# Kernel tuning notes

Hardware: AMD Instinct MI355X
Metric: run time of the kernel (lower is better)

Reference implementation:

```python
import jax, jax.numpy as jnp
import numpy as np

# Longformer-base-4096 dims; attention_window=128 -> one-sided window 64
B, S, D, H, L, F, V, NUM_LABELS = 1, 4096, 768, 12, 12, 3072, 50265, 100
DH = D // H
W = 64            # one-sided sliding window
NC = S // W       # number of query chunks
EPS = 1e-5
SCALE = float(1.0 / np.sqrt(DH))


def layer_norm(x, s, b):
    m = jnp.mean(x, axis=-1, keepdims=True)
    v = jnp.mean(jnp.square(x - m), axis=-1, keepdims=True)
    return (x - m) * jax.lax.rsqrt(v + EPS) * s + b


def heads(x):  # [B,S,D] -> [B,H,S,DH]
    return x.reshape(B, S, H, DH).transpose(0, 2, 1, 3)


def chunk3(t):  # [B,H,S,DH] -> [B,H,NC,3W,DH]: key blocks c-1,c,c+1 per query chunk c
    tp = jnp.pad(t, ((0, 0), (0, 0), (W, W), (0, 0)))
    tb = tp.reshape(B, H, NC + 2, W, DH)
    return jnp.concatenate([tb[:, :, i:i + NC] for i in range(3)], axis=3)


def _forward(input_ids, attention_mask, emb_tok, emb_pos, ln_emb_scale, ln_emb_bias,
             Wq, bq, Wk, bk, Wv, bv, Wqg, bqg, Wkg, bkg, Wvg, bvg, Wo, bo,
             ln1_scale, ln1_bias, Wf1, bf1, Wf2, bf2, ln2_scale, ln2_bias, Wc, bc):
    am = attention_mask > 0                      # [B,S]
    x = layer_norm(emb_tok[input_ids] + emb_pos[None, :, :], ln_emb_scale, ln_emb_bias)

    # static sliding-window masks, shared by all layers
    qi = jnp.arange(W)[:, None]
    kj = jnp.arange(3 * W)[None, :]
    band = (kj >= qi) & (kj <= qi + 2 * W)       # |key - query| <= W within a chunk triple
    kvalid = am & (jnp.arange(S)[None, :] > 0)   # global token (pos 0) excluded from window
    kp = jnp.pad(kvalid, ((0, 0), (W, W))).reshape(B, NC + 2, W)
    kmask = jnp.concatenate([kp[:, i:i + NC] for i in range(3)], axis=2)   # [B,NC,3W]
    win_mask = band[None, None, None] & kmask[:, None, :, None, :]         # [B,1,NC,W,3W]

    def layer(x, p):
        (wq, bq_, wk, bk_, wv, bv_, wqg, bqg_, wkg, bkg_, wvg, bvg_, wo, bo_,
         l1s, l1b, wf1, bf1_, wf2, bf2_, l2s, l2b) = p
        q = heads(x @ wq + bq_) * SCALE
        k = heads(x @ wk + bk_)
        v = heads(x @ wv + bv_)
        qc = q.reshape(B, H, NC, W, DH)
        k3, v3 = chunk3(k), chunk3(v)
        sc = jnp.einsum('bhcqd,bhckd->bhcqk', qc, k3)          # [B,H,NC,W,3W]
        sc = jnp.where(win_mask, sc, -1e9)
        # every token also attends to the global CLS key (standard K/V of pos 0)
        sg = jnp.einsum('bhsd,bhd->bhs', q, k[:, :, 0]).reshape(B, H, NC, W, 1)
        probs = jax.nn.softmax(jnp.concatenate([sg, sc], axis=-1), axis=-1)
        pg, pl = probs[..., 0], probs[..., 1:]
        ctx = jnp.einsum('bhcqk,bhckd->bhcqd', pl, v3).reshape(B, H, S, DH)
        ctx = ctx + pg.reshape(B, H, S, 1) * v[:, :, :1]
        # global token attends to everything with its own (global) projections
        qg = heads(x @ wqg + bqg_)[:, :, 0] * SCALE            # [B,H,DH]
        kg = heads(x @ wkg + bkg_)
        vg = heads(x @ wvg + bvg_)
        sgl = jnp.where(am[:, None, :], jnp.einsum('bhd,bhjd->bhj', qg, kg), -1e9)
        ctx0 = jnp.einsum('bhj,bhjd->bhd', jax.nn.softmax(sgl, axis=-1), vg)
        ctx = ctx.at[:, :, 0].set(ctx0)
        attn = ctx.transpose(0, 2, 1, 3).reshape(B, S, D) @ wo + bo_
        x1 = layer_norm(x + attn, l1s, l1b)
        h = jax.nn.gelu(x1 @ wf1 + bf1_, approximate=False)
        return layer_norm(x1 + h @ wf2 + bf2_, l2s, l2b), None

    params = (Wq, bq, Wk, bk, Wv, bv, Wqg, bqg, Wkg, bkg, Wvg, bvg, Wo, bo,
              ln1_scale, ln1_bias, Wf1, bf1, Wf2, bf2, ln2_scale, ln2_bias)
    x, _ = jax.lax.scan(layer, x, params)
    return x[:, 0] @ Wc + bc                                   # [B, NUM_LABELS]


def setup_inputs():
    key = jax.random.key(0)
    ks = jax.random.split(key, 40)
    it = iter(range(40))
    nrm = lambda shape: jax.random.normal(ks[next(it)], shape, dtype=jnp.float32) * 0.02
    z = lambda shape: jnp.zeros(shape, jnp.float32)
    o = lambda shape: jnp.ones(shape, jnp.float32)
    return {
        'input_ids': jax.random.randint(ks[next(it)], (B, S), 0, V, dtype=jnp.int32),
        'attention_mask': jnp.ones((B, S), dtype=jnp.int32),
        'emb_tok': nrm((V, D)), 'emb_pos': nrm((S, D)),
        'ln_emb_scale': o((D,)), 'ln_emb_bias': z((D,)),
        'Wq': nrm((L, D, D)), 'bq': z((L, D)),
        'Wk': nrm((L, D, D)), 'bk': z((L, D)),
        'Wv': nrm((L, D, D)), 'bv': z((L, D)),
        'Wqg': nrm((L, D, D)), 'bqg': z((L, D)),
        'Wkg': nrm((L, D, D)), 'bkg': z((L, D)),
        'Wvg': nrm((L, D, D)), 'bvg': z((L, D)),
        'Wo': nrm((L, D, D)), 'bo': z((L, D)),
        'ln1_scale': o((L, D)), 'ln1_bias': z((L, D)),
        'Wf1': nrm((L, D, F)), 'bf1': z((L, F)),
        'Wf2': nrm((L, F, D)), 'bf2': z((L, D)),
        'ln2_scale': o((L, D)), 'ln2_bias': z((L, D)),
        'Wc': nrm((D, NUM_LABELS)), 'bc': z((NUM_LABELS,)),
    }


def reference(input_ids, attention_mask, emb_tok, emb_pos, ln_emb_scale, ln_emb_bias,
              Wq, bq, Wk, bk, Wv, bv, Wqg, bqg, Wkg, bkg, Wvg, bvg, Wo, bo,
              ln1_scale, ln1_bias, Wf1, bf1, Wf2, bf2, ln2_scale, ln2_bias, Wc, bc):
    return _forward(input_ids, attention_mask, emb_tok, emb_pos, ln_emb_scale, ln_emb_bias,
                    Wq, bq, Wk, bk, Wv, bv, Wqg, bqg, Wkg, bkg, Wvg, bvg, Wo, bo,
                    ln1_scale, ln1_bias, Wf1, bf1, Wf2, bf2, ln2_scale, ln2_bias, Wc, bc)
```

## Files before the change

kernel.cpp:

```cpp
#include <hip/hip_runtime.h>
#include <hip/hip_bf16.h>

typedef unsigned short u16;
typedef __attribute__((ext_vector_type(8))) short bf16x8;
typedef __attribute__((ext_vector_type(4))) float f32x4;

constexpr int S = 4096, D = 768, H = 12, NL = 12, F = 3072, NLAB = 100, DH = 64;
constexpr int NQKV = 3840;
constexpr float SCALE = 0.125f;
constexpr float EPS = 1e-5f;

__device__ __forceinline__ float bits2f(u16 u) {
  union { unsigned int i; float f; } x; x.i = ((unsigned int)u) << 16; return x.f;
}
__device__ __forceinline__ u16 f2bbits(float f) {
  union { float f; unsigned int i; } x; x.f = f;
  return (u16)((x.i + 0x7FFFu + ((x.i >> 16) & 1u)) >> 16);
}
__device__ __forceinline__ float rdw(const void* p, size_t i, int isf32) {
  return isf32 ? ((const float*)p)[i] : bits2f(((const u16*)p)[i]);
}
__device__ __forceinline__ void gload16(const void* g, void* l) {
  __builtin_amdgcn_global_load_lds(
      (const __attribute__((address_space(1))) void*)g,
      (__attribute__((address_space(3))) void*)l, 16, 0, 0);
}

__global__ void detect_k(const void* lns, int* flag) {
  *flag = (*(const unsigned int*)lns == 0x3F800000u) ? 1 : 0;
}

struct PrepArgs {
  const void *Wq, *Wk, *Wv, *Wkg, *Wvg, *Wo, *Wqg, *Wf1, *Wf2;
  const void *bq, *bk, *bv, *bkg, *bvg, *bo, *bqg, *bf1, *bf2;
  u16 *wt_qkv, *wt_o, *wt_qg, *wt_f1, *wt_f2;
  float* biasb;
  const int* flag;
};

__global__ __launch_bounds__(256) void prep_all(PrepArgs a)
{
  const int l = blockIdx.x / 8676;
  const int b = blockIdx.x % 8676;
  const int t = threadIdx.x;
  const int isf32 = *a.flag;
  const size_t oDD = (size_t)l * D * D, oDF = (size_t)l * D * F;
  const size_t oD = (size_t)l * D, oF = (size_t)l * F;
  u16* wqkv = a.wt_qkv + (size_t)l * NQKV * D;
  u16* wo   = a.wt_o   + (size_t)l * D * D;
  u16* wqg  = a.wt_qg  + (size_t)l * D * D;
  u16* wf1  = a.wt_f1  + (size_t)l * F * D;
  u16* wf2  = a.wt_f2  + (size_t)l * D * F;
  float* bb = a.biasb + (size_t)l * 9216;

  if (b < 8640) {
    __shared__ float tile[32][33];
    const void* src; size_t soff; int N, ld, rowoff, n0, k0;
    u16* dst; float scl = 1.f;
    if (b < 4032) {
      const int m = b / 576, ti = b - m * 576;
      soff = oDD; N = D; ld = D; rowoff = 0;
      switch (m) {
        case 0:  src = a.Wq;  dst = wqkv; scl = SCALE;  break;
        case 1:  src = a.Wk;  dst = wqkv; rowoff = 768; break;
        case 2:  src = a.Wv;  dst = wqkv; rowoff = 1536; break;
        case 3:  src = a.Wkg; dst = wqkv; rowoff = 2304; break;
        case 4:  src = a.Wvg; dst = wqkv; rowoff = 3072; break;
        case 5:  src = a.Wo;  dst = wo;   break;
        default: src = a.Wqg; dst = wqg;  scl = SCALE;  break;
      }
      n0 = (ti % 24) * 32; k0 = (ti / 24) * 32;
    } else if (b < 6336) {
      const int ti = b - 4032;
      src = a.Wf1; soff = oDF; N = F; dst = wf1; rowoff = 0; ld = D;
      n0 = (ti % 96) * 32; k0 = (ti / 96) * 32;
    } else {
      const int ti = b - 6336;
      src = a.Wf2; soff = oDF; N = D; dst = wf2; rowoff = 0; ld = F;
      n0 = (ti % 24) * 32; k0 = (ti / 24) * 32;
    }
    const int r = t >> 3, cc = (t & 7) << 2;
    const size_t si = soff + (size_t)(k0 + r) * N + n0 + cc;
    if (isf32) {
      const float4 v = *reinterpret_cast<const float4*>(&((const float*)src)[si]);
      tile[r][cc] = v.x * scl; tile[r][cc+1] = v.y * scl;
      tile[r][cc+2] = v.z * scl; tile[r][cc+3] = v.w * scl;
    } else {
      const ushort4 v = *reinterpret_cast<const ushort4*>(&((const u16*)src)[si]);
      tile[r][cc] = bits2f(v.x) * scl; tile[r][cc+1] = bits2f(v.y) * scl;
      tile[r][cc+2] = bits2f(v.z) * scl; tile[r][cc+3] = bits2f(v.w) * scl;
    }
    __syncthreads();
    const ushort4 ov = make_ushort4(f2bbits(tile[cc+0][r]), f2bbits(tile[cc+1][r]),
                                    f2bbits(tile[cc+2][r]), f2bbits(tile[cc+3][r]));
    *reinterpret_cast<ushort4*>(&dst[(size_t)(rowoff + n0 + r) * ld + k0 + cc]) = ov;
  } else {
    const int i = (b - 8640) * 256 + t;
    float v;
    if      (i < 768)  v = rdw(a.bq,  oD + i,        isf32) * SCALE;
    else if (i < 1536) v = rdw(a.bk,  oD + i - 768,  isf32);
    else if (i < 2304) v = rdw(a.bv,  oD + i - 1536, isf32);
    else if (i < 3072) v = rdw(a.bkg, oD + i - 2304, isf32);
    else if (i < 3840) v = rdw(a.bvg, oD + i - 3072, isf32);
    else if (i < 4608) v = rdw(a.bo,  oD + i - 3840, isf32);
    else if (i < 7680) v = rdw(a.bf1, oF + i - 4608, isf32);
    else if (i < 8448) v = rdw(a.bf2, oD + i - 7680, isf32);
    else               v = rdw(a.bqg, oD + i - 8448, isf32) * SCALE;
    bb[i] = v;
  }
}

template<int BN, int SPLITK>
__global__ __launch_bounds__(256) void mfma_gemm(
    const u16* __restrict__ A, const u16* __restrict__ BT,
    const float* __restrict__ bias,
    float* __restrict__ Cf, u16* __restrict__ Cb,
    int M, int N, int K, int act)
{
  constexpr int BM = 128, BK = 32;
  constexpr int WN = BN / 2;
  constexpr int NR = WN / 16;
  __shared__ u16 As[BM * BK];
  __shared__ u16 Bs[BN * BK];
  const int t = threadIdx.x;
  const int wid = t >> 6, lane = t & 63;
  const int wr = wid >> 1, wc = wid & 1;
  const int m0 = blockIdx.y * BM, n0 = blockIdx.x * BN;
  const int z = (SPLITK > 1) ? blockIdx.z : 0;
  const int kLen = K / SPLITK;
  const int k0 = z * kLen;
  const int l_row = lane >> 2;
  const int l_kc = (lane & 3) << 3;

  f32x4 acc[4][NR];
#pragma unroll
  for (int m = 0; m < 4; ++m)
#pragma unroll
    for (int n = 0; n < NR; ++n)
      acc[m][n] = (f32x4){0.f, 0.f, 0.f, 0.f};

  const int frow = lane & 15;
  const int fkb = (lane >> 4) << 3;

  for (int kt = k0; kt < k0 + kLen; kt += BK) {
#pragma unroll
    for (int i = 0; i < 2; ++i) {
      const int ch = wid * 2 + i;
      gload16(&A[(size_t)(m0 + ch * 16 + l_row) * K + kt + l_kc], &As[ch * 512]);
    }
#pragma unroll
    for (int i = 0; i < BN / 64; ++i) {
      const int ch = wid * (BN / 64) + i;
      gload16(&BT[(size_t)(n0 + ch * 16 + l_row) * K + kt + l_kc], &Bs[ch * 512]);
    }
    __syncthreads();
    bf16x8 af[4], bfr[NR];
#pragma unroll
    for (int m = 0; m < 4; ++m)
      af[m] = *reinterpret_cast<const bf16x8*>(&As[(wr * 64 + m * 16 + frow) * BK + fkb]);
#pragma unroll
    for (int n = 0; n < NR; ++n)
      bfr[n] = *reinterpret_cast<const bf16x8*>(&Bs[(wc * WN + n * 16 + frow) * BK + fkb]);
#pragma unroll
    for (int m = 0; m < 4; ++m)
#pragma unroll
      for (int n = 0; n < NR; ++n)
        acc[m][n] = __builtin_amdgcn_mfma_f32_16x16x32_bf16(af[m], bfr[n], acc[m][n], 0, 0, 0);
    __syncthreads();
  }

  float* Cp = (SPLITK > 1) ? (Cf + (size_t)z * M * N) : Cf;
  const int crow = (lane >> 4) << 2;
  const int ccol = lane & 15;
#pragma unroll
  for (int m = 0; m < 4; ++m) {
#pragma unroll
    for (int n = 0; n < NR; ++n) {
      const int gc = n0 + wc * WN + n * 16 + ccol;
      const float bv = (z == 0) ? bias[gc] : 0.f;
#pragma unroll
      for (int r = 0; r < 4; ++r) {
        const int gr = m0 + wr * 64 + m * 16 + crow + r;
        float x = acc[m][n][r] + bv;
        if (SPLITK == 1 && act) x = 0.5f * x * (1.0f + erff(x * 0.70710678118654752f));
        if (Cp) Cp[(size_t)gr * N + gc] = x;
        if (SPLITK == 1 && Cb) Cb[(size_t)gr * N + gc] = f2bbits(x);
      }
    }
  }
}

__global__ void embed_k(const int* __restrict__ ids, const void* __restrict__ tok,
                        const void* __restrict__ pos, float* __restrict__ out,
                        const int* __restrict__ flag)
{
  const int isf32 = *flag;
  const int s = blockIdx.x, t = threadIdx.x;
  const int id = ids[s];
  for (int c = t; c < D; c += 256)
    out[(size_t)s * D + c] = rdw(tok, (size_t)id * D + c, isf32) + rdw(pos, (size_t)s * D + c, isf32);
}

__global__ __launch_bounds__(256) void ln_res_k(
    const float* __restrict__ Ain,
    const float* __restrict__ P0, const float* __restrict__ P1,
    const float* __restrict__ P2, const float* __restrict__ P3,
    const void* __restrict__ g, size_t goff, const void* __restrict__ b, size_t boff,
    float* __restrict__ Out, u16* __restrict__ Outb, const int* __restrict__ flag)
{
  const int isf32 = *flag;
  const int w = threadIdx.x >> 6, lane = threadIdx.x & 63;
  const int r = blockIdx.x * 4 + w;
  const size_t rb = (size_t)r * D;
  float v[12];
  float ls = 0.f;
#pragma unroll
  for (int j = 0; j < 3; ++j) {
    const int c = lane * 4 + j * 256;
    float4 x = *reinterpret_cast<const float4*>(&Ain[rb + c]);
    if (P0) { const float4 p = *reinterpret_cast<const float4*>(&P0[rb + c]);
              x.x += p.x; x.y += p.y; x.z += p.z; x.w += p.w; }
    if (P1) { const float4 p = *reinterpret_cast<const float4*>(&P1[rb + c]);
              x.x += p.x; x.y += p.y; x.z += p.z; x.w += p.w; }
    if (P2) { const float4 p = *reinterpret_cast<const float4*>(&P2[rb + c]);
              x.x += p.x; x.y += p.y; x.z += p.z; x.w += p.w; }
    if (P3) { const float4 p = *reinterpret_cast<const float4*>(&P3[rb + c]);
              x.x += p.x; x.y += p.y; x.z += p.z; x.w += p.w; }
    v[j*4+0] = x.x; v[j*4+1] = x.y; v[j*4+2] = x.z; v[j*4+3] = x.w;
    ls += x.x + x.y + x.z + x.w;
  }
#pragma unroll
  for (int off = 32; off; off >>= 1) ls += __shfl_xor(ls, off);
  const float mean = ls * (1.0f / D);
  float lv = 0.f;
#pragma unroll
  for (int e = 0; e < 12; ++e) { const float dd = v[e] - mean; lv += dd * dd; }
#pragma unroll
  for (int off = 32; off; off >>= 1) lv += __shfl_xor(lv, off);
  const float rstd = rsqrtf(lv * (1.0f / D) + EPS);
#pragma unroll
  for (int j = 0; j < 3; ++j) {
    const int c = lane * 4 + j * 256;
    float o[4];
#pragma unroll
    for (int e = 0; e < 4; ++e)
      o[e] = (v[j*4+e] - mean) * rstd * rdw(g, goff + c + e, isf32) + rdw(b, boff + c + e, isf32);
    *reinterpret_cast<float4*>(&Out[rb + c]) = make_float4(o[0], o[1], o[2], o[3]);
    if (Outb)
      *reinterpret_cast<ushort4*>(&Outb[rb + c]) =
          make_ushort4(f2bbits(o[0]), f2bbits(o[1]), f2bbits(o[2]), f2bbits(o[3]));
  }
}

__global__ __launch_bounds__(256) void qg_gemv(
    const u16* __restrict__ Xb, const u16* __restrict__ WgT,
    const float* __restrict__ biasb, float* __restrict__ QG)
{
  const int wid = threadIdx.x >> 6, lane = threadIdx.x & 63;
  const int o = blockIdx.x * 4 + wid;
  float a = 0.f;
#pragma unroll
  for (int j = 0; j < 12; ++j) {
    const int k = j * 64 + lane;
    a += bits2f(Xb[k]) * bits2f(WgT[(size_t)o * 768 + k]);
  }
#pragma unroll
  for (int off = 32; off; off >>= 1) a += __shfl_xor(a, off);
  if (lane == 0) QG[o] = a + biasb[8448 + o];
}

__global__ __launch_bounds__(256) void win_attn3(
    const u16* __restrict__ QKV, const int* __restrict__ am, u16* __restrict__ CTXb)
{
  __shared__ u16 Ql[64 * 64];
  __shared__ u16 Kl[224 * 64];
  __shared__ u16 Vt[64 * 232];
  __shared__ int kwin[224];
  const int c = blockIdx.x, h = blockIdx.y;
  const int t = threadIdx.x, w = t >> 6, lane = t & 63;
  const int base = c * 64 - 64, s0 = c * 64;

  for (int i = t; i < 1024; i += 256) {
    const int r = i >> 4, c4 = (i & 15) << 2;
    const ushort4 v = *reinterpret_cast<const ushort4*>(
        &QKV[(size_t)(s0 + r) * NQKV + h * 64 + c4]);
    *reinterpret_cast<ushort4*>((char*)Ql + ((r * 128 + c4 * 2) ^ ((r & 7) << 4))) = v;
  }
  for (int i = t; i < 3584; i += 256) {
    const int r = i >> 4, c4 = (i & 15) << 2;
    const int kp = (r < 192) ? (base + r) : ((r == 192) ? 0 : -1);
    ushort4 v = make_ushort4(0, 0, 0, 0);
    if (kp >= 0 && kp < S)
      v = *reinterpret_cast<const ushort4*>(&QKV[(size_t)kp * NQKV + 768 + h * 64 + c4]);
    *reinterpret_cast<ushort4*>((char*)Kl + ((r * 128 + c4 * 2) ^ ((r & 7) << 4))) = v;
  }
  for (int i = t; i < 3584; i += 256) {
    const int r = i >> 4, c4 = (i & 15) << 2;
    const int kp = (r < 192) ? (base + r) : ((r == 192) ? 0 : -1);
    ushort4 v = make_ushort4(0, 0, 0, 0);
    if (kp >= 0 && kp < S)
      v = *reinterpret_cast<const ushort4*>(&QKV[(size_t)kp * NQKV + 1536 + h * 64 + c4]);
    Vt[(c4 + 0) * 232 + r] = v.x;
    Vt[(c4 + 1) * 232 + r] = v.y;
    Vt[(c4 + 2) * 232 + r] = v.z;
    Vt[(c4 + 3) * 232 + r] = v.w;
  }
  if (t < 224) {
    const int kp = base + t;
    kwin[t] = (t < 192 && kp >= 1 && kp < S) ? am[kp] : 0;
  }
  __syncthreads();

  const int frow = lane & 15, fkb = (lane >> 4) << 3;
  const int crow = (lane >> 4) << 2, ccol = lane & 15;
  const int qrow = w * 16 + frow;

  bf16x8 aq[2];
#pragma unroll
  for (int ks = 0; ks < 2; ++ks)
    aq[ks] = *reinterpret_cast<const bf16x8*>(
        (const char*)Ql + ((qrow * 128 + (ks * 32 + fkb) * 2) ^ ((qrow & 7) << 4)));

  f32x4 sc[14];
#pragma unroll
  for (int tl = 0; tl < 14; ++tl) {
    sc[tl] = (f32x4){0.f, 0.f, 0.f, 0.f};
    const int key = tl * 16 + frow;
#pragma unroll
    for (int ks = 0; ks < 2; ++ks) {
      const bf16x8 bk = *reinterpret_cast<const bf16x8*>(
          (const char*)Kl + ((key * 128 + (ks * 32 + fkb) * 2) ^ ((key & 7) << 4)));
      sc[tl] = __builtin_amdgcn_mfma_f32_16x16x32_bf16(aq[ks], bk, sc[tl], 0, 0, 0);
    }
  }

  float m4[4] = {-1e30f, -1e30f, -1e30f, -1e30f};
#pragma unroll
  for (int tl = 0; tl < 14; ++tl) {
    const int kidx = tl * 16 + ccol;
    const int kw = kwin[kidx];
    const bool isg = (kidx == 192);
#pragma unroll
    for (int r = 0; r < 4; ++r) {
      const int qi = w * 16 + crow + r;
      const bool valid = isg || ((kidx >= qi) && (kidx <= qi + 128) && kw);
      const float v = valid ? sc[tl][r] : -1e30f;
      sc[tl][r] = v;
      m4[r] = fmaxf(m4[r], v);
    }
  }
#pragma unroll
  for (int r = 0; r < 4; ++r)
#pragma unroll
    for (int off = 8; off; off >>= 1) m4[r] = fmaxf(m4[r], __shfl_xor(m4[r], off));

  float ssum[4] = {0.f, 0.f, 0.f, 0.f};
#pragma unroll
  for (int tl = 0; tl < 14; ++tl)
#pragma unroll
    for (int r = 0; r < 4; ++r) {
      const float e = __expf(sc[tl][r] - m4[r]);
      sc[tl][r] = e;
      ssum[r] += e;
    }
#pragma unroll
  for (int r = 0; r < 4; ++r)
#pragma unroll
    for (int off = 8; off; off >>= 1) ssum[r] += __shfl_xor(ssum[r], off);

  __syncthreads();
  u16* Pl = Kl;
#pragma unroll
  for (int tl = 0; tl < 14; ++tl) {
    const int kidx = tl * 16 + ccol;
#pragma unroll
    for (int r = 0; r < 4; ++r) {
      const int row = crow + r;
      *(u16*)((char*)Pl + w * 7168 + ((row * 448 + kidx * 2) ^ ((row & 7) << 4))) =
          f2bbits(sc[tl][r]);
    }
  }
  __syncthreads();

  bf16x8 pa[7];
#pragma unroll
  for (int ks = 0; ks < 7; ++ks)
    pa[ks] = *reinterpret_cast<const bf16x8*>(
        (const char*)Pl + w * 7168 + ((frow * 448 + (ks * 32 + fkb) * 2) ^ ((frow & 7) << 4)));

  f32x4 av[4];
#pragma unroll
  for (int n = 0; n < 4; ++n) {
    av[n] = (f32x4){0.f, 0.f, 0.f, 0.f};
#pragma unroll
    for (int ks = 0; ks < 7; ++ks) {
      const bf16x8 bv = *reinterpret_cast<const bf16x8*>(&Vt[(n * 16 + frow) * 232 + ks * 32 + fkb]);
      av[n] = __builtin_amdgcn_mfma_f32_16x16x32_bf16(pa[ks], bv, av[n], 0, 0, 0);
    }
  }
  float inv[4];
#pragma unroll
  for (int r = 0; r < 4; ++r) inv[r] = 1.f / ssum[r];
#pragma unroll
  for (int n = 0; n < 4; ++n)
#pragma unroll
    for (int r = 0; r < 4; ++r) {
      const int s = s0 + w * 16 + crow + r;
      CTXb[(size_t)s * D + h * 64 + n * 16 + ccol] = f2bbits(av[n][r] * inv[r]);
    }
}

__global__ __launch_bounds__(256) void glob_part(
    const u16* __restrict__ QKV, const float* __restrict__ QG,
    const int* __restrict__ am, float* __restrict__ gp)
{
  __shared__ float qsh[DH];
  __shared__ float se[256];
  __shared__ float red[4];
  __shared__ float part[4][DH];
  const int seg = blockIdx.x, h = blockIdx.y, t = threadIdx.x;
  const int j0 = seg * 256;
  if (t < DH) qsh[t] = QG[h * DH + t];
  __syncthreads();
  const int j = j0 + t;
  float a = 0.f;
  const u16* kr = &QKV[(size_t)j * NQKV + 2304 + h * 64];
#pragma unroll
  for (int v8 = 0; v8 < 8; ++v8) {
    const bf16x8 kv = *reinterpret_cast<const bf16x8*>(&kr[v8 * 8]);
#pragma unroll
    for (int e = 0; e < 8; ++e)
      a += qsh[v8 * 8 + e] * bits2f((u16)kv[e]);
  }
  a = (am[j] > 0) ? a : -1e9f;
  float m = a;
#pragma unroll
  for (int off = 32; off; off >>= 1) m = fmaxf(m, __shfl_xor(m, off));
  if ((t & 63) == 0) red[t >> 6] = m;
  __syncthreads();
  m = fmaxf(fmaxf(red[0], red[1]), fmaxf(red[2], red[3]));
  const float e = __expf(a - m);
  se[t] = e;
  float ls = e;
#pragma unroll
  for (int off = 32; off; off >>= 1) ls += __shfl_xor(ls, off);
  __syncthreads();
  if ((t & 63) == 0) red[t >> 6] = ls;
  __syncthreads();
  const float lsum = red[0] + red[1] + red[2] + red[3];
  const int g = t >> 6, d = t & 63;
  float acc = 0.f;
  for (int jj = g; jj < 256; jj += 4)
    acc += se[jj] * bits2f(QKV[(size_t)(j0 + jj) * NQKV + 3072 + h * 64 + d]);
  part[g][d] = acc;
  __syncthreads();
  if (t < 64) {
    float* o = &gp[(size_t)(h * 16 + seg) * 66];
    o[t] = part[0][t] + part[1][t] + part[2][t] + part[3][t];
    if (t == 0) { o[64] = m; o[65] = lsum; }
  }
}

__global__ void glob_comb(const float* __restrict__ gp, u16* __restrict__ CTXb)
{
  const int h = blockIdx.x, t = threadIdx.x;
  float M = -1e30f;
  for (int i = 0; i < 16; ++i) M = fmaxf(M, gp[(size_t)(h * 16 + i) * 66 + 64]);
  float L = 0.f, acc = 0.f;
  for (int i = 0; i < 16; ++i) {
    const float* o = &gp[(size_t)(h * 16 + i) * 66];
    const float w = __expf(o[64] - M);
    L += o[65] * w;
    acc += o[t] * w;
  }
  CTXb[h * 64 + t] = f2bbits(acc / L);
}

__global__ __launch_bounds__(256) void cls_k(
    const float* __restrict__ X, const void* __restrict__ Wc,
    const void* __restrict__ bc, void* __restrict__ out,
    const int* __restrict__ flag)
{
  const int isf32 = *flag;
  const int wid = threadIdx.x >> 6, lane = threadIdx.x & 63;
  const int n = blockIdx.x * 4 + wid;
  if (n >= NLAB) return;
  float a = 0.f;
#pragma unroll
  for (int j = 0; j < 12; ++j) {
    const int k = j * 64 + lane;
    a += X[k] * rdw(Wc, (size_t)k * NLAB + n, isf32);
  }
#pragma unroll
  for (int off = 32; off; off >>= 1) a += __shfl_xor(a, off);
  if (lane == 0) {
    a += rdw(bc, n, isf32);
    if (isf32) ((float*)out)[n] = a;
    else ((u16*)out)[n] = f2bbits(a);
  }
}

extern "C" void kernel_launch(void* const* d_in, const int* in_sizes, int n_in,
                              void* d_out, int out_size, void* d_ws, size_t ws_size,
                              hipStream_t stream)
{
  const int*  ids = (const int*)d_in[0];
  const int*  am  = (const int*)d_in[1];
  const void* emb_tok = d_in[2];
  const void* emb_pos = d_in[3];
  const void* ln_e_g  = d_in[4];
  const void* ln_e_b  = d_in[5];
  const void* Wq  = d_in[6];  const void* bq  = d_in[7];
  const void* Wk  = d_in[8];  const void* bk  = d_in[9];
  const void* Wv  = d_in[10]; const void* bv  = d_in[11];
  const void* Wqg = d_in[12]; const void* bqg = d_in[13];
  const void* Wkg = d_in[14]; const void* bkg = d_in[15];
  const void* Wvg = d_in[16]; const void* bvg = d_in[17];
  const void* Wo  = d_in[18]; const void* bo  = d_in[19];
  const void* l1g = d_in[20]; const void* l1b = d_in[21];
  const void* Wf1 = d_in[22]; const void* bf1 = d_in[23];
  const void* Wf2 = d_in[24]; const void* bf2 = d_in[25];
  const void* l2g = d_in[26]; const void* l2b = d_in[27];
  const void* Wc  = d_in[28]; const void* bc  = d_in[29];

  float* ws = (float*)d_ws;
  const size_t SD = (size_t)S * D;
  size_t cur = 0;
  auto af32 = [&](size_t n) { float* p = ws + cur; cur += n; return p; };
  auto au16 = [&](size_t n_u16) { u16* p = (u16*)(ws + cur); cur += (n_u16 + 1) / 2; return p; };

  float* X     = af32(SD);
  float* X1    = af32(SD);
  float* TMP   = af32(2 * SD);
  u16*   QKV16 = au16(5 * SD);
  u16*   Hb    = au16((size_t)S * F);
  u16*   Xb    = au16(SD);
  u16*   X1b   = au16(SD);
  u16*   CTXb  = au16(SD);
  u16*   wt_qkv = au16((size_t)NL * NQKV * D);
  u16*   wt_o   = au16((size_t)NL * D * D);
  u16*   wt_qg  = au16((size_t)NL * D * D);
  u16*   wt_f1  = au16((size_t)NL * F * D);
  u16*   wt_f2  = au16((size_t)NL * D * F);
  float* biasb  = af32((size_t)NL * 9216);
  float* QGb    = af32(768);
  float* gp     = af32((size_t)H * 16 * 66);
  int*   flag   = (int*)af32(4);

  float* T0 = TMP;
  float* T1 = TMP + SD;

  detect_k<<<1, 1, 0, stream>>>(ln_e_g, flag);

  PrepArgs pa;
  pa.Wq = Wq; pa.Wk = Wk; pa.Wv = Wv; pa.Wkg = Wkg; pa.Wvg = Wvg;
  pa.Wo = Wo; pa.Wqg = Wqg; pa.Wf1 = Wf1; pa.Wf2 = Wf2;
  pa.bq = bq; pa.bk = bk; pa.bv = bv; pa.bkg = bkg; pa.bvg = bvg;
  pa.bo = bo; pa.bqg = bqg; pa.bf1 = bf1; pa.bf2 = bf2;
  pa.wt_qkv = wt_qkv; pa.wt_o = wt_o; pa.wt_qg = wt_qg;
  pa.wt_f1 = wt_f1; pa.wt_f2 = wt_f2; pa.biasb = biasb; pa.flag = flag;
  prep_all<<<NL * 8676, 256, 0, stream>>>(pa);

  embed_k<<<S, 256, 0, stream>>>(ids, emb_tok, emb_pos, T0, flag);
  ln_res_k<<<S / 4, 256, 0, stream>>>(T0, nullptr, nullptr, nullptr, nullptr,
                                      ln_e_g, 0, ln_e_b, 0, X, Xb, flag);

  for (int l = 0; l < NL; ++l) {
    const size_t oD = (size_t)l * D;
    u16* wqkv_l = wt_qkv + (size_t)l * NQKV * D;
    u16* wo_l   = wt_o   + (size_t)l * D * D;
    u16* wqg_l  = wt_qg  + (size_t)l * D * D;
    u16* wf1_l  = wt_f1  + (size_t)l * F * D;
    u16* wf2_l  = wt_f2  + (size_t)l * D * F;
    float* bb_l = biasb + (size_t)l * 9216;

    mfma_gemm<128, 1><<<dim3(NQKV / 128, S / 128), 256, 0, stream>>>(
        Xb, wqkv_l, bb_l, nullptr, QKV16, S, NQKV, D, 0);
    qg_gemv<<<192, 256, 0, stream>>>(Xb, wqg_l, bb_l, QGb);
    win_attn3<<<dim3(S / 64, H), 256, 0, stream>>>(QKV16, am, CTXb);
    glob_part<<<dim3(16, H), 256, 0, stream>>>(QKV16, QGb, am, gp);
    glob_comb<<<H, 64, 0, stream>>>(gp, CTXb);
    mfma_gemm<64, 2><<<dim3(D / 64, S / 128, 2), 256, 0, stream>>>(
        CTXb, wo_l, bb_l + 3840, TMP, nullptr, S, D, D, 0);
    ln_res_k<<<S / 4, 256, 0, stream>>>(X, T0, T1, nullptr, nullptr,
                                        l1g, oD, l1b, oD, X1, X1b, flag);
    mfma_gemm<128, 1><<<dim3(F / 128, S / 128), 256, 0, stream>>>(
        X1b, wf1_l, bb_l + 4608, nullptr, Hb, S, F, D, 1);
    mfma_gemm<64, 2><<<dim3(D / 64, S / 128, 2), 256, 0, stream>>>(
        Hb, wf2_l, bb_l + 7680, TMP, nullptr, S, D, F, 0);
    ln_res_k<<<S / 4, 256, 0, stream>>>(X1, T0, T1, nullptr, nullptr,
                                        l2g, oD, l2b, oD, X, Xb, flag);
  }
  cls_k<<<25, 256, 0, stream>>>(X, Wc, bc, d_out, flag);
}
```

Baseline: 3.104 ms.

## Add 256x256 triple-buffered MFMA GEMM for QKV and FFN-up projections

Introduces a new 512-thread GEMM kernel with 256x256 output tiles, triple-buffered LDS staging via direct global-to-LDS loads, and raised wave priority around the MFMA block. It replaces the 128x128 kernel for the QKV projection and the FFN up-projection with GELU. Larger tiles cut global/LDS traffic per flop, but the grids shrink (15x16 and 12x16 blocks), which may underfill the 256 CUs, and register pressure from 32 accumulators is high. It also drops the unused residual inputs from the layer-norm kernel and tidies up the prep kernel.

```diff
diff --git a/kernel.cpp b/kernel.cpp
--- a/kernel.cpp
+++ b/kernel.cpp
@@ -37,20 +37,16 @@
   float* biasb;
   const int* flag;
 };
+constexpr int PPL = 8676;
 
 __global__ __launch_bounds__(256) void prep_all(PrepArgs a)
 {
-  const int l = blockIdx.x / 8676;
-  const int b = blockIdx.x % 8676;
+  const int l = blockIdx.x / PPL;
+  const int b = blockIdx.x % PPL;
   const int t = threadIdx.x;
   const int isf32 = *a.flag;
   const size_t oDD = (size_t)l * D * D, oDF = (size_t)l * D * F;
   const size_t oD = (size_t)l * D, oF = (size_t)l * F;
-  u16* wqkv = a.wt_qkv + (size_t)l * NQKV * D;
-  u16* wo   = a.wt_o   + (size_t)l * D * D;
-  u16* wqg  = a.wt_qg  + (size_t)l * D * D;
-  u16* wf1  = a.wt_f1  + (size_t)l * F * D;
-  u16* wf2  = a.wt_f2  + (size_t)l * D * F;
   float* bb = a.biasb + (size_t)l * 9216;
 
   if (b < 8640) {
@@ -61,22 +57,22 @@
       const int m = b / 576, ti = b - m * 576;
       soff = oDD; N = D; ld = D; rowoff = 0;
       switch (m) {
-        case 0:  src = a.Wq;  dst = wqkv; scl = SCALE;  break;
-        case 1:  src = a.Wk;  dst = wqkv; rowoff = 768; break;
-        case 2:  src = a.Wv;  dst = wqkv; rowoff = 1536; break;
-        case 3:  src = a.Wkg; dst = wqkv; rowoff = 2304; break;
-        case 4:  src = a.Wvg; dst = wqkv; rowoff = 3072; break;
-        case 5:  src = a.Wo;  dst = wo;   break;
-        default: src = a.Wqg; dst = wqg;  scl = SCALE;  break;
+        case 0:  src = a.Wq;  dst = a.wt_qkv + (size_t)l * NQKV * D; scl = SCALE;  break;
+        case 1:  src = a.Wk;  dst = a.wt_qkv + (size_t)l * NQKV * D; rowoff = 768; break;
+        case 2:  src = a.Wv;  dst = a.wt_qkv + (size_t)l * NQKV * D; rowoff = 1536; break;
+        case 3:  src = a.Wkg; dst = a.wt_qkv + (size_t)l * NQKV * D; rowoff = 2304; break;
+        case 4:  src = a.Wvg; dst = a.wt_qkv + (size_t)l * NQKV * D; rowoff = 3072; break;
+        case 5:  src = a.Wo;  dst = a.wt_o   + (size_t)l * D * D;    break;
+        default: src = a.Wqg; dst = a.wt_qg  + (size_t)l * D * D;    scl = SCALE;  break;
       }
       n0 = (ti % 24) * 32; k0 = (ti / 24) * 32;
     } else if (b < 6336) {
       const int ti = b - 4032;
-      src = a.Wf1; soff = oDF; N = F; dst = wf1; rowoff = 0; ld = D;
+      src = a.Wf1; soff = oDF; N = F; dst = a.wt_f1 + (size_t)l * F * D; rowoff = 0; ld = D;
       n0 = (ti % 96) * 32; k0 = (ti / 96) * 32;
     } else {
       const int ti = b - 6336;
-      src = a.Wf2; soff = oDF; N = D; dst = wf2; rowoff = 0; ld = F;
+      src = a.Wf2; soff = oDF; N = D; dst = a.wt_f2 + (size_t)l * D * F; rowoff = 0; ld = F;
       n0 = (ti % 24) * 32; k0 = (ti / 24) * 32;
     }
     const int r = t >> 3, cc = (t & 7) << 2;
@@ -110,6 +106,96 @@
   }
 }
 
+__global__ __launch_bounds__(512) void gemm256(
+    const u16* __restrict__ A, const u16* __restrict__ BT,
+    const float* __restrict__ bias, u16* __restrict__ Cb,
+    int M, int N, int K, int act)
+{
+  __shared__ u16 smem[49152];
+  const int t = threadIdx.x;
+  const int wid = t >> 6, lane = t & 63;
+  const int wm = wid >> 2, wn = wid & 3;
+  const int m0 = blockIdx.y * 256, n0 = blockIdx.x * 256;
+  const int nt = K >> 5;
+
+  const int srow = lane >> 2;
+  const int skc = (lane & 3) << 3;
+
+  auto stage = [&](int kt, int b) {
+#pragma unroll
+    for (int j = 0; j < 4; ++j) {
+      const int half = j & 1;
+      const int row = half * 128 + wid * 16 + srow;
+      const u16* src = (j < 2)
+          ? &A [(size_t)(m0 + row) * K + kt * 32 + skc]
+          : &BT[(size_t)(n0 + row) * K + kt * 32 + skc];
+      gload16(src, &smem[b * 16384 + (j >= 2 ? 8192 : 0) + half * 4096 + wid * 512]);
+    }
+  };
+
+  f32x4 acc[8][4];
+#pragma unroll
+  for (int mf = 0; mf < 8; ++mf)
+#pragma unroll
+    for (int nf = 0; nf < 4; ++nf)
+      acc[mf][nf] = (f32x4){0.f, 0.f, 0.f, 0.f};
+
+  const int frow = lane & 15;
+  const int fkb = (lane >> 4) << 3;
+
+  stage(0, 0);
+  stage(1, 1);
+  asm volatile("s_waitcnt vmcnt(4)" ::: "memory");
+  __builtin_amdgcn_s_barrier();
+
+  for (int kt = 0; kt < nt; ++kt) {
+    const int rb = (kt % 3) * 16384;
+    bf16x8 Af[8], Bf[4];
+#pragma unroll
+    for (int mf = 0; mf < 8; ++mf)
+      Af[mf] = *reinterpret_cast<const bf16x8*>(
+          &smem[rb + (wm * 128 + mf * 16 + frow) * 32 + fkb]);
+#pragma unroll
+    for (int nf = 0; nf < 4; ++nf)
+      Bf[nf] = *reinterpret_cast<const bf16x8*>(
+          &smem[rb + 8192 + (wn * 64 + nf * 16 + frow) * 32 + fkb]);
+
+    if (kt + 2 < nt) stage(kt + 2, (kt + 2) % 3);
+
+    asm volatile("s_waitcnt lgkmcnt(0)" ::: "memory");
+    __builtin_amdgcn_sched_barrier(0);
+    __builtin_amdgcn_s_setprio(1);
+#pragma unroll
+    for (int mf = 0; mf < 8; ++mf)
+#pragma unroll
+      for (int nf = 0; nf < 4; ++nf)
+        acc[mf][nf] = __builtin_amdgcn_mfma_f32_16x16x32_bf16(Af[mf], Bf[nf], acc[mf][nf], 0, 0, 0);
+    __builtin_amdgcn_s_setprio(0);
+
+    if (kt < nt - 2)       asm volatile("s_waitcnt vmcnt(4)" ::: "memory");
+    else if (kt == nt - 2) asm volatile("s_waitcnt vmcnt(0)" ::: "memory");
+    __builtin_amdgcn_s_barrier();
+  }
+
+  const int crow = (lane >> 4) << 2;
+  const int ccol = lane & 15;
+#pragma unroll
+  for (int mf = 0; mf < 8; ++mf) {
+#pragma unroll
+    for (int nf = 0; nf < 4; ++nf) {
+      const int gc = n0 + wn * 64 + nf * 16 + ccol;
+      const float bv = bias[gc];
+#pragma unroll
+      for (int r = 0; r < 4; ++r) {
+        const int gr = m0 + wm * 128 + mf * 16 + crow + r;
+        float x = acc[mf][nf][r] + bv;
+        if (act) x = 0.5f * x * (1.0f + erff(x * 0.70710678118654752f));
+        Cb[(size_t)gr * N + gc] = f2bbits(x);
+      }
+    }
+  }
+}
+
 template<int BN, int SPLITK>
 __global__ __launch_bounds__(256) void mfma_gemm(
     const u16* __restrict__ A, const u16* __restrict__ BT,
@@ -204,7 +290,6 @@
 __global__ __launch_bounds__(256) void ln_res_k(
     const float* __restrict__ Ain,
     const float* __restrict__ P0, const float* __restrict__ P1,
-    const float* __restrict__ P2, const float* __restrict__ P3,
     const void* __restrict__ g, size_t goff, const void* __restrict__ b, size_t boff,
     float* __restrict__ Out, u16* __restrict__ Outb, const int* __restrict__ flag)
 {
@@ -221,10 +306,6 @@
     if (P0) { const float4 p = *reinterpret_cast<const float4*>(&P0[rb + c]);
               x.x += p.x; x.y += p.y; x.z += p.z; x.w += p.w; }
     if (P1) { const float4 p = *reinterpret_cast<const float4*>(&P1[rb + c]);
-              x.x += p.x; x.y += p.y; x.z += p.z; x.w += p.w; }
-    if (P2) { const float4 p = *reinterpret_cast<const float4*>(&P2[rb + c]);
-              x.x += p.x; x.y += p.y; x.z += p.z; x.w += p.w; }
-    if (P3) { const float4 p = *reinterpret_cast<const float4*>(&P3[rb + c]);
               x.x += p.x; x.y += p.y; x.z += p.z; x.w += p.w; }
     v[j*4+0] = x.x; v[j*4+1] = x.y; v[j*4+2] = x.z; v[j*4+3] = x.w;
     ls += x.x + x.y + x.z + x.w;
@@ -559,10 +640,10 @@
   pa.bo = bo; pa.bqg = bqg; pa.bf1 = bf1; pa.bf2 = bf2;
   pa.wt_qkv = wt_qkv; pa.wt_o = wt_o; pa.wt_qg = wt_qg;
   pa.wt_f1 = wt_f1; pa.wt_f2 = wt_f2; pa.biasb = biasb; pa.flag = flag;
-  prep_all<<<NL * 8676, 256, 0, stream>>>(pa);
+  prep_all<<<NL * PPL, 256, 0, stream>>>(pa);
 
   embed_k<<<S, 256, 0, stream>>>(ids, emb_tok, emb_pos, T0, flag);
-  ln_res_k<<<S / 4, 256, 0, stream>>>(T0, nullptr, nullptr, nullptr, nullptr,
+  ln_res_k<<<S / 4, 256, 0, stream>>>(T0, nullptr, nullptr,
                                       ln_e_g, 0, ln_e_b, 0, X, Xb, flag);
 
   for (int l = 0; l < NL; ++l) {
@@ -574,21 +655,21 @@
     u16* wf2_l  = wt_f2  + (size_t)l * D * F;
     float* bb_l = biasb + (size_t)l * 9216;
 
-    mfma_gemm<128, 1><<<dim3(NQKV / 128, S / 128), 256, 0, stream>>>(
-        Xb, wqkv_l, bb_l, nullptr, QKV16, S, NQKV, D, 0);
+    gemm256<<<dim3(NQKV / 256, S / 256), 512, 0, stream>>>(
+        Xb, wqkv_l, bb_l, QKV16, S, NQKV, D, 0);
     qg_gemv<<<192, 256, 0, stream>>>(Xb, wqg_l, bb_l, QGb);
     win_attn3<<<dim3(S / 64, H), 256, 0, stream>>>(QKV16, am, CTXb);
     glob_part<<<dim3(16, H), 256, 0, stream>>>(QKV16, QGb, am, gp);
     glob_comb<<<H, 64, 0, stream>>>(gp, CTXb);
     mfma_gemm<64, 2><<<dim3(D / 64, S / 128, 2), 256, 0, stream>>>(
         CTXb, wo_l, bb_l + 3840, TMP, nullptr, S, D, D, 0);
-    ln_res_k<<<S / 4, 256, 0, stream>>>(X, T0, T1, nullptr, nullptr,
+    ln_res_k<<<S / 4, 256, 0, stream>>>(X, T0, T1,
                                         l1g, oD, l1b, oD, X1, X1b, flag);
-    mfma_gemm<128, 1><<<dim3(F / 128, S / 128), 256, 0, stream>>>(
-        X1b, wf1_l, bb_l + 4608, nullptr, Hb, S, F, D, 1);
+    gemm256<<<dim3(F / 256, S / 256), 512, 0, stream>>>(
+        X1b, wf1_l, bb_l + 4608, Hb, S, F, D, 1);
     mfma_gemm<64, 2><<<dim3(D / 64, S / 128, 2), 256, 0, stream>>>(
         Hb, wf2_l, bb_l + 7680, TMP, nullptr, S, D, F, 0);
-    ln_res_k<<<S / 4, 256, 0, stream>>>(X1, T0, T1, nullptr, nullptr,
+    ln_res_k<<<S / 4, 256, 0, stream>>>(X1, T0, T1,
                                         l2g, oD, l2b, oD, X, Xb, flag);
   }
   cls_k<<<25, 256, 0, stream>>>(X, Wc, bc, d_out, flag);
```

Result: no change. 3.097 ms (median of 2 runs) (-0.2%).
